# Kernel tuning notes

Hardware: AMD Instinct MI355X
Metric: run time of the kernel (lower is better)

The kernel has to match this reference:

```python
import jax, jax.numpy as jnp
import numpy as np

V, E, H, S, L = 32000, 512, 1024, 512, 256


def _cell(x, h, c, Wih, Whh, bih, bhh):
    # PyTorch LSTM cell, gate order i, f, g, o
    gates = Wih @ x + bih + Whh @ h + bhh
    i, f, g, o = jnp.split(gates, 4)
    c2 = jax.nn.sigmoid(f) * c + jax.nn.sigmoid(i) * jnp.tanh(g)
    h2 = jax.nn.sigmoid(o) * jnp.tanh(c2)
    return h2, c2


def setup_inputs() -> dict:
    key = jax.random.key(0)
    ks = jax.random.split(key, 24)
    s = 0.03  # ~1/sqrt(H), like torch LSTM default init scale
    def n(k, shape, scale=s):
        return jax.random.normal(k, shape, dtype=jnp.float32) * scale
    return {
        "x": jax.random.randint(ks[0], (S,), 0, V),
        "y": jax.random.randint(ks[1], (L,), 0, V),
        "emb": n(ks[2], (V, E)),
        "enc_Wih0": n(ks[3], (4 * H, E)), "enc_Whh0": n(ks[4], (4 * H, H)),
        "enc_bih0": n(ks[5], (4 * H,)), "enc_bhh0": n(ks[6], (4 * H,)),
        "enc_Wih1": n(ks[7], (4 * H, H)), "enc_Whh1": n(ks[8], (4 * H, H)),
        "enc_bih1": n(ks[9], (4 * H,)), "enc_bhh1": n(ks[10], (4 * H,)),
        "enc_fcW": n(ks[11], (H, H)), "enc_fcb": n(ks[12], (H,)),
        # decoder input is the raw token id as a float; scale its input weight
        # by ~1/V so gate pre-activations stay O(1)
        "dec_Wih0": n(ks[13], (4 * H, 1), 1.0 / V), "dec_Whh0": n(ks[14], (4 * H, H)),
        "dec_bih0": n(ks[15], (4 * H,)), "dec_bhh0": n(ks[16], (4 * H,)),
        "dec_Wih1": n(ks[17], (4 * H, H)), "dec_Whh1": n(ks[18], (4 * H, H)),
        "dec_bih1": n(ks[19], (4 * H,)), "dec_bhh1": n(ks[20], (4 * H,)),
        "dec_fcW": n(ks[21], (V, H)), "dec_fcb": n(ks[22], (V,)),
    }


def reference(x, y, emb, enc_Wih0, enc_Whh0, enc_bih0, enc_bhh0,
              enc_Wih1, enc_Whh1, enc_bih1, enc_bhh1, enc_fcW, enc_fcb,
              dec_Wih0, dec_Whh0, dec_bih0, dec_bhh0,
              dec_Wih1, dec_Whh1, dec_bih1, dec_bhh1, dec_fcW, dec_fcb):
    h_dim = enc_Whh0.shape[1]
    vocab = dec_fcW.shape[0]

    # ---- Encoder: 2-layer LSTM over the noisy sequence, batch=1 ----
    emb_seq = emb[x]  # [S, E]

    def enc_step(carry, e_t):
        h0, c0, h1, c1 = carry
        h0, c0 = _cell(e_t, h0, c0, enc_Wih0, enc_Whh0, enc_bih0, enc_bhh0)
        h1, c1 = _cell(h0, h1, c1, enc_Wih1, enc_Whh1, enc_bih1, enc_bhh1)
        return (h0, c0, h1, c1), None

    z = jnp.zeros((h_dim,), jnp.float32)
    (_, _, h1, _), _ = jax.lax.scan(enc_step, (z, z, z, z), emb_seq)
    lat = jax.nn.relu(enc_fcW @ h1 + enc_fcb)       # [H] (latent == hidden)
    h_s0 = jnp.stack([lat, lat])                    # replicated across layers

    # ---- Decoder: free-running greedy decode (tfr=0.0) ----
    # Faithful quirk: each step re-initializes the cell state to the hidden
    # state (original passes (h_s_enc, h_s_enc) every call).
    def dec_step(carry, _):
        x_f, h = carry
        h0n, _ = _cell(jnp.reshape(x_f, (1,)), h[0], h[0],
                       dec_Wih0, dec_Whh0, dec_bih0, dec_bhh0)
        h1n, _ = _cell(h0n, h[1], h[1],
                       dec_Wih1, dec_Whh1, dec_bih1, dec_bhh1)
        logits = dec_fcW @ h1n + dec_fcb            # [V]
        x_next = jnp.argmax(logits).astype(jnp.float32)
        return (x_next, jnp.stack([h0n, h1n])), logits

    x0 = y[0].astype(jnp.float32)
    _, logits_seq = jax.lax.scan(dec_step, (x0, h_s0), None, length=y.shape[0] - 1)
    # outputs[0] stays zeros, as in the original
    return jnp.concatenate([jnp.zeros((1, vocab), jnp.float32), logits_seq], axis=0)
```

## Files before the change

kernel.cpp:

```cpp
#include <hip/hip_runtime.h>
#include <hip/hip_bf16.h>

typedef unsigned short u16;
typedef unsigned int   u32;

#define NB    256
#define NT    512
#define HD    1024
#define G4    4096
#define VOCAB 32000
#define EDIM  512
#define SLEN  512
#define RPB   (VOCAB / NB)

__device__ __forceinline__ float bflo(u32 u){ union{u32 i; float f;} v; v.i = u << 16; return v.f; }
__device__ __forceinline__ float bfhi(u32 u){ union{u32 i; float f;} v; v.i = u & 0xffff0000u; return v.f; }
__device__ __forceinline__ float bf1(u16 u){ union{u32 i; float f;} v; v.i = ((u32)u) << 16; return v.f; }
__device__ __forceinline__ u16 f2bf(float f){
    union{float f; u32 i;} v; v.f = f;
    u32 x = v.i;
    u32 r = (x + 0x7fffu + ((x >> 16) & 1u)) >> 16;
    return (u16)r;
}

__device__ __forceinline__ float sigm(float x){ return 1.f / (1.f + __expf(-x)); }
__device__ __forceinline__ float tanh_f(float x){ float e = __expf(2.f * x); return 1.f - 2.f / (e + 1.f); }

__device__ __forceinline__ float wave_sum(float v){
#pragma unroll
    for (int off = 32; off > 0; off >>= 1) v += __shfl_xor(v, off, 64);
    return v;
}

__device__ __forceinline__ float dot16bf(uint4 a, uint4 b, const float* h){
    float s = 0.f;
    s = fmaf(bflo(a.x), h[0],  s); s = fmaf(bfhi(a.x), h[1],  s);
    s = fmaf(bflo(a.y), h[2],  s); s = fmaf(bfhi(a.y), h[3],  s);
    s = fmaf(bflo(a.z), h[4],  s); s = fmaf(bfhi(a.z), h[5],  s);
    s = fmaf(bflo(a.w), h[6],  s); s = fmaf(bfhi(a.w), h[7],  s);
    s = fmaf(bflo(b.x), h[8],  s); s = fmaf(bfhi(b.x), h[9],  s);
    s = fmaf(bflo(b.y), h[10], s); s = fmaf(bfhi(b.y), h[11], s);
    s = fmaf(bflo(b.z), h[12], s); s = fmaf(bfhi(b.z), h[13], s);
    s = fmaf(bflo(b.w), h[14], s); s = fmaf(bfhi(b.w), h[15], s);
    return s;
}

__device__ __forceinline__ void load16(const float* src, int lane, float* d){
    const float4* p = (const float4*)(src + (lane << 4));
    float4 a = p[0], b = p[1], c = p[2], e = p[3];
    d[0]=a.x; d[1]=a.y; d[2]=a.z; d[3]=a.w;
    d[4]=b.x; d[5]=b.y; d[6]=b.z; d[7]=b.w;
    d[8]=c.x; d[9]=c.y; d[10]=c.z; d[11]=c.w;
    d[12]=e.x; d[13]=e.y; d[14]=e.z; d[15]=e.w;
}

struct TBF {
    static __device__ __forceinline__ float g(const void* p, int i){ return bf1(((const u16*)p)[i]); }
    static __device__ __forceinline__ const void* rp(const void* p, size_t eoff){ return (const void*)((const u16*)p + eoff); }
    static __device__ __forceinline__ float dot1024(const void* pr, const float* h, int lane){
        const u16* row = (const u16*)pr;
        const uint4* p = (const uint4*)(row + ((size_t)lane << 4));
        uint4 a = p[0], b = p[1];
        return dot16bf(a, b, h);
    }
    static __device__ __forceinline__ float dot512(const void* pr, const float* h8, int lane){
        const u16* row = (const u16*)pr;
        uint4 a = *((const uint4*)(row + ((size_t)lane << 3)));
        float s = 0.f;
        s = fmaf(bflo(a.x), h8[0], s); s = fmaf(bfhi(a.x), h8[1], s);
        s = fmaf(bflo(a.y), h8[2], s); s = fmaf(bfhi(a.y), h8[3], s);
        s = fmaf(bflo(a.z), h8[4], s); s = fmaf(bfhi(a.z), h8[5], s);
        s = fmaf(bflo(a.w), h8[6], s); s = fmaf(bfhi(a.w), h8[7], s);
        return s;
    }
    static __device__ __forceinline__ void vec8(const void* pr, int lane, float* d){
        const u16* src = (const u16*)pr;
        uint4 a = *((const uint4*)(src + ((size_t)lane << 3)));
        d[0]=bflo(a.x); d[1]=bfhi(a.x); d[2]=bflo(a.y); d[3]=bfhi(a.y);
        d[4]=bflo(a.z); d[5]=bfhi(a.z); d[6]=bflo(a.w); d[7]=bfhi(a.w);
    }
    static __device__ __forceinline__ void store(void* o, size_t i, float v){ ((u16*)o)[i] = f2bf(v); }
    static __device__ __forceinline__ void zero(void* o, size_t i){ ((u16*)o)[i] = 0; }
};

struct TF32 {
    static __device__ __forceinline__ float g(const void* p, int i){ return ((const float*)p)[i]; }
    static __device__ __forceinline__ const void* rp(const void* p, size_t eoff){ return (const void*)((const float*)p + eoff); }
    static __device__ __forceinline__ float dot1024(const void* pr, const float* h, int lane){
        const float4* p = (const float4*)((const float*)pr + ((size_t)lane << 4));
        float4 a = p[0], b = p[1], c = p[2], e = p[3];
        float s = 0.f;
        s = fmaf(a.x, h[0],  s); s = fmaf(a.y, h[1],  s); s = fmaf(a.z, h[2],  s); s = fmaf(a.w, h[3],  s);
        s = fmaf(b.x, h[4],  s); s = fmaf(b.y, h[5],  s); s = fmaf(b.z, h[6],  s); s = fmaf(b.w, h[7],  s);
        s = fmaf(c.x, h[8],  s); s = fmaf(c.y, h[9],  s); s = fmaf(c.z, h[10], s); s = fmaf(c.w, h[11], s);
        s = fmaf(e.x, h[12], s); s = fmaf(e.y, h[13], s); s = fmaf(e.z, h[14], s); s = fmaf(e.w, h[15], s);
        return s;
    }
    static __device__ __forceinline__ float dot512(const void* pr, const float* h8, int lane){
        const float4* p = (const float4*)((const float*)pr + ((size_t)lane << 3));
        float4 a = p[0], b = p[1];
        float s = 0.f;
        s = fmaf(a.x, h8[0], s); s = fmaf(a.y, h8[1], s); s = fmaf(a.z, h8[2], s); s = fmaf(a.w, h8[3], s);
        s = fmaf(b.x, h8[4], s); s = fmaf(b.y, h8[5], s); s = fmaf(b.z, h8[6], s); s = fmaf(b.w, h8[7], s);
        return s;
    }
    static __device__ __forceinline__ void vec8(const void* pr, int lane, float* d){
        const float4* p = (const float4*)((const float*)pr + ((size_t)lane << 3));
        float4 a = p[0], b = p[1];
        d[0]=a.x; d[1]=a.y; d[2]=a.z; d[3]=a.w;
        d[4]=b.x; d[5]=b.y; d[6]=b.z; d[7]=b.w;
    }
    static __device__ __forceinline__ void store(void* o, size_t i, float v){ ((float*)o)[i] = v; }
    static __device__ __forceinline__ void zero(void* o, size_t i){ ((float*)o)[i] = 0.f; }
};

__device__ __forceinline__ void grid_barrier(u32* bar, u32 tgen, int bid){
    __syncthreads();
    if (threadIdx.x == 0){
        __builtin_amdgcn_fence(__ATOMIC_RELEASE, "agent");
        u32 a = __hip_atomic_fetch_add(&bar[(bid & 7) * 32], 1u,
                                       __ATOMIC_RELAXED, __HIP_MEMORY_SCOPE_AGENT);
        if ((a % 32u) == 31u){
            u32 m = __hip_atomic_fetch_add(&bar[256], 1u,
                                           __ATOMIC_RELAXED, __HIP_MEMORY_SCOPE_AGENT);
            if ((m % 8u) == 7u)
                __hip_atomic_store(&bar[288], tgen, __ATOMIC_RELAXED, __HIP_MEMORY_SCOPE_AGENT);
        }
        while (__hip_atomic_load(&bar[288], __ATOMIC_RELAXED, __HIP_MEMORY_SCOPE_AGENT) < tgen)
            __builtin_amdgcn_s_sleep(1);
        __builtin_amdgcn_fence(__ATOMIC_ACQUIRE, "agent");
    }
    __syncthreads();
}

__global__ void ws_init(u32* ws){
    int i = threadIdx.x + blockIdx.x * blockDim.x;
    if (i < 1024) ws[i] = 0u;
}

__global__ void dtype_probe(const u16* emb, u32* ws){
    __shared__ int sh[4];
    int tid = threadIdx.x;
    int bad = 0;
    for (int i = tid; i < 2048; i += 256){
        u32 e = ((u32)emb[i] >> 7) & 0xFFu;
        if (e >= 0x82u) bad++;
    }
#pragma unroll
    for (int off = 32; off > 0; off >>= 1) bad += __shfl_xor(bad, off, 64);
    if ((tid & 63) == 0) sh[tid >> 6] = bad;
    __syncthreads();
    if (tid == 0){
        int t = sh[0] + sh[1] + sh[2] + sh[3];
        ws[512] = (t > 8) ? 1u : 0u;
    }
}

template<class W, u32 WANT>
__global__ __launch_bounds__(NT) void dae_main(
    const int* __restrict__ xs, const int* __restrict__ ys,
    const void* __restrict__ emb,
    const void* __restrict__ eWih0, const void* __restrict__ eWhh0,
    const void* __restrict__ ebih0, const void* __restrict__ ebhh0,
    const void* __restrict__ eWih1, const void* __restrict__ eWhh1,
    const void* __restrict__ ebih1, const void* __restrict__ ebhh1,
    const void* __restrict__ efcW,  const void* __restrict__ efcb,
    const void* __restrict__ dWih0, const void* __restrict__ dWhh0,
    const void* __restrict__ dbih0, const void* __restrict__ dbhh0,
    const void* __restrict__ dWih1, const void* __restrict__ dWhh1,
    const void* __restrict__ dbih1, const void* __restrict__ dbhh1,
    const void* __restrict__ dfcW,  const void* __restrict__ dfcb,
    void* __restrict__ out, u32* __restrict__ ws)
{
    if (__hip_atomic_load(&ws[512], __ATOMIC_RELAXED, __HIP_MEMORY_SCOPE_AGENT) != WANT) return;

    const int tid  = threadIdx.x;
    const int bid  = blockIdx.x;
    const int lane = tid & 63;
    const int wave = tid >> 6;

    __shared__ __align__(16) float h0s[HD];
    __shared__ __align__(16) float h1s[HD];
    __shared__ float redmax[8];
    __shared__ int   redidx[8];
    __shared__ float xf_sh;

    u32*   bar  = ws;
    float* G0   = (float*)(ws + 1024);
    float* G1   = G0 + 2 * G4;
    float* M0   = G1 + 2 * G4;
    float* Fv   = M0 + 2 * G4;
    float* bmax = Fv + HD;
    int*   bidxv= (int*)(bmax + NB);

    u32 phase = 0;
    float c0r[2] = {0.f, 0.f};
    float c1r[2] = {0.f, 0.f};

    for (int i = tid; i < HD; i += NT){ h0s[i] = 0.f; h1s[i] = 0.f; }
    for (int i = tid; i < RPB; i += NT) W::zero(out, (size_t)bid * RPB + i);

    {
        int tok = xs[0];
        float er[8];
        W::vec8(W::rp(emb, (size_t)tok * EDIM), lane, er);
        const int rb = bid * 16 + wave * 2;
#pragma unroll
        for (int i = 0; i < 2; ++i){
            int r = rb + i;
            float s = W::dot512(W::rp(eWih0, (size_t)r * EDIM), er, lane);
            s = wave_sum(s);
            if (lane == 0) G0[r] = s + W::g(ebih0, r) + W::g(ebhh0, r);
        }
    }
    grid_barrier(bar, ++phase, bid);

    for (int t = 0; t < SLEN; ++t){
        const int cur = t & 1, nxt = cur ^ 1;
        if (t >= 1){
            const float* Gg = G1 + nxt * G4;
#pragma unroll
            for (int i = 0; i < 2; ++i){
                int r = tid * 2 + i;
                float ig = Gg[r], fg = Gg[r + HD], gg = Gg[r + 2*HD], og = Gg[r + 3*HD];
                float c = sigm(fg) * c1r[i] + sigm(ig) * tanh_f(gg);
                c1r[i] = c;
                h1s[r] = sigm(og) * tanh_f(c);
            }
        }
        {
            const float* Gg = G0 + cur * G4;
#pragma unroll
            for (int i = 0; i < 2; ++i){
                int r = tid * 2 + i;
                float ig = Gg[r], fg = Gg[r + HD], gg = Gg[r + 2*HD], og = Gg[r + 3*HD];
                float c = sigm(fg) * c0r[i] + sigm(ig) * tanh_f(gg);
                c0r[i] = c;
                h0s[r] = sigm(og) * tanh_f(c);
            }
        }
        __syncthreads();
        float h0r[16], h1r[16];
        load16(h0s, lane, h0r);
        load16(h1s, lane, h1r);
        const int rb = bid * 16 + wave * 2;
        if (t < SLEN - 1){
            int tok = xs[t + 1];
            float er[8];
            W::vec8(W::rp(emb, (size_t)tok * EDIM), lane, er);
#pragma unroll
            for (int i = 0; i < 2; ++i){
                int r = rb + i;
                float s = W::dot1024(W::rp(eWhh0, (size_t)r * HD), h0r, lane)
                        + W::dot512(W::rp(eWih0, (size_t)r * EDIM), er, lane);
                s = wave_sum(s);
                if (lane == 0) G0[nxt * G4 + r] = s + W::g(ebih0, r) + W::g(ebhh0, r);
            }
        }
#pragma unroll
        for (int i = 0; i < 2; ++i){
            int r = rb + i;
            float s = W::dot1024(W::rp(eWih1, (size_t)r * HD), h0r, lane)
                    + W::dot1024(W::rp(eWhh1, (size_t)r * HD), h1r, lane);
            s = wave_sum(s);
            if (lane == 0) G1[cur * G4 + r] = s + W::g(ebih1, r) + W::g(ebhh1, r);
        }
        grid_barrier(bar, ++phase, bid);
    }

    {
        const float* Gg = G1 + ((SLEN - 1) & 1) * G4;
#pragma unroll
        for (int i = 0; i < 2; ++i){
            int r = tid * 2 + i;
            float ig = Gg[r], fg = Gg[r + HD], gg = Gg[r + 2*HD], og = Gg[r + 3*HD];
            float c = sigm(fg) * c1r[i] + sigm(ig) * tanh_f(gg);
            c1r[i] = c;
            h1s[r] = sigm(og) * tanh_f(c);
        }
        __syncthreads();
        float h1r[16];
        load16(h1s, lane, h1r);
        if (wave < 4){
            int r = bid * 4 + wave;
            float s = W::dot1024(W::rp(efcW, (size_t)r * HD), h1r, lane);
            s = wave_sum(s);
            if (lane == 0) Fv[r] = s + W::g(efcb, r);
        }
        grid_barrier(bar, ++phase, bid);
    }

    {
        for (int i = tid; i < HD; i += NT){
            float v = Fv[i]; v = v > 0.f ? v : 0.f;
            h0s[i] = v; h1s[i] = v;
        }
        __syncthreads();
        float h0r[16];
        load16(h0s, lane, h0r);
        const int rb = bid * 16 + wave * 2;
#pragma unroll
        for (int i = 0; i < 2; ++i){
            int r = rb + i;
            float s = W::dot1024(W::rp(dWhh0, (size_t)r * HD), h0r, lane);
            s = wave_sum(s);
            if (lane == 0) M0[G4 + r] = s + W::g(dbih0, r) + W::g(dbhh0, r);
        }
        grid_barrier(bar, ++phase, bid);
    }

    for (int t = 1; t < 256; ++t){
        float xf;
        if (t == 1){
            xf = (float)ys[0];
        } else {
            if (wave == 0){
                float m = bmax[lane]; int mi = bidxv[lane];
#pragma unroll
                for (int j = 64; j < NB; j += 64){
                    float m2 = bmax[lane + j]; int i2 = bidxv[lane + j];
                    if (m2 > m || (m2 == m && i2 < mi)){ m = m2; mi = i2; }
                }
#pragma unroll
                for (int off = 32; off > 0; off >>= 1){
                    float m2 = __shfl_xor(m, off, 64);
                    int   i2 = __shfl_xor(mi, off, 64);
                    if (m2 > m || (m2 == m && i2 < mi)){ m = m2; mi = i2; }
                }
                if (lane == 0) xf_sh = (float)mi;
            }
            __syncthreads();
            xf = xf_sh;
        }
        {
            const float* Gg = M0 + (t & 1) * G4;
#pragma unroll
            for (int i = 0; i < 2; ++i){
                int r = tid * 2 + i;
                float ig = Gg[r]        + xf * W::g(dWih0, r);
                float fg = Gg[r + HD]   + xf * W::g(dWih0, r + HD);
                float gg = Gg[r + 2*HD] + xf * W::g(dWih0, r + 2*HD);
                float og = Gg[r + 3*HD] + xf * W::g(dWih0, r + 3*HD);
                float cp = h0s[r];
                float c  = sigm(fg) * cp + sigm(ig) * tanh_f(gg);
                h0s[r]   = sigm(og) * tanh_f(c);
            }
        }
        __syncthreads();
        {
            float h0r[16], h1r[16];
            load16(h0s, lane, h0r);
            load16(h1s, lane, h1r);
            const int rb = bid * 16 + wave * 2;
#pragma unroll
            for (int i = 0; i < 2; ++i){
                int r = rb + i;
                float s1 = W::dot1024(W::rp(dWih1, (size_t)r * HD), h0r, lane)
                         + W::dot1024(W::rp(dWhh1, (size_t)r * HD), h1r, lane);
                s1 = wave_sum(s1);
                if (lane == 0) G1[(t & 1) * G4 + r] = s1 + W::g(dbih1, r) + W::g(dbhh1, r);
                float s0 = W::dot1024(W::rp(dWhh0, (size_t)r * HD), h0r, lane);
                s0 = wave_sum(s0);
                if (lane == 0) M0[((t + 1) & 1) * G4 + r] = s0 + W::g(dbih0, r) + W::g(dbhh0, r);
            }
        }
        grid_barrier(bar, ++phase, bid);

        {
            const float* Gg = G1 + (t & 1) * G4;
#pragma unroll
            for (int i = 0; i < 2; ++i){
                int r = tid * 2 + i;
                float ig = Gg[r], fg = Gg[r + HD], gg = Gg[r + 2*HD], og = Gg[r + 3*HD];
                float cp = h1s[r];
                float c  = sigm(fg) * cp + sigm(ig) * tanh_f(gg);
                h1s[r]   = sigm(og) * tanh_f(c);
            }
        }
        __syncthreads();
        {
            float h1r[16];
            load16(h1s, lane, h1r);
            float wmax = -3.4e38f; int wmi = 0x7fffffff;
            for (int i = wave; i < RPB; i += 8){
                int r = bid * RPB + i;
                float s = W::dot1024(W::rp(dfcW, (size_t)r * HD), h1r, lane);
                s = wave_sum(s) + W::g(dfcb, r);
                if (lane == 0) W::store(out, (size_t)t * VOCAB + r, s);
                if (s > wmax){ wmax = s; wmi = r; }
            }
            if (lane == 0){ redmax[wave] = wmax; redidx[wave] = wmi; }
        }
        __syncthreads();
        if (tid == 0){
            float m = redmax[0]; int mi = redidx[0];
#pragma unroll
            for (int w = 1; w < 8; ++w){
                if (redmax[w] > m || (redmax[w] == m && redidx[w] < mi)){ m = redmax[w]; mi = redidx[w]; }
            }
            bmax[bid] = m; bidxv[bid] = mi;
        }
        grid_barrier(bar, ++phase, bid);
    }
}

extern "C" void kernel_launch(void* const* d_in, const int* in_sizes, int n_in,
                              void* d_out, int out_size, void* d_ws, size_t ws_size,
                              hipStream_t stream) {
    const int* xs = (const int*)d_in[0];
    const int* ys = (const int*)d_in[1];
    u32* ws = (u32*)d_ws;

    ws_init<<<4, 256, 0, stream>>>(ws);
    dtype_probe<<<1, 256, 0, stream>>>((const u16*)d_in[2], ws);

    dae_main<TBF, 0u><<<NB, NT, 0, stream>>>(
        xs, ys, d_in[2],
        d_in[3], d_in[4], d_in[5], d_in[6], d_in[7], d_in[8], d_in[9], d_in[10],
        d_in[11], d_in[12],
        d_in[13], d_in[14], d_in[15], d_in[16], d_in[17], d_in[18], d_in[19], d_in[20],
        d_in[21], d_in[22],
        d_out, ws);
    dae_main<TF32, 1u><<<NB, NT, 0, stream>>>(
        xs, ys, d_in[2],
        d_in[3], d_in[4], d_in[5], d_in[6], d_in[7], d_in[8], d_in[9], d_in[10],
        d_in[11], d_in[12],
        d_in[13], d_in[14], d_in[15], d_in[16], d_in[17], d_in[18], d_in[19], d_in[20],
        d_in[21], d_in[22],
        d_out, ws);
}
```

Baseline: 16.08 ms.

## Replace barrier acquire fence with agent-scope atomic loads and unroll vocab projection

Drops the acquire fence in the grid barrier, which invalidates caches. All cross-block shared buffers (gate pre-activations, latent, argmax partials) are instead read and written with relaxed agent-scope atomic loads and stores so they stay coherent. The vocab projection loop is also unrolled by two rows per wave to overlap two dot products. Correctness now relies on every cross-block access going through the atomic helpers. A missed access, or compiler reordering without the fence, could read stale data.

```diff
diff --git a/kernel.cpp b/kernel.cpp
--- a/kernel.cpp
+++ b/kernel.cpp
@@ -25,6 +25,19 @@
 
 __device__ __forceinline__ float sigm(float x){ return 1.f / (1.f + __expf(-x)); }
 __device__ __forceinline__ float tanh_f(float x){ float e = __expf(2.f * x); return 1.f - 2.f / (e + 1.f); }
+
+__device__ __forceinline__ float gldf(const float* p){
+    return __hip_atomic_load(p, __ATOMIC_RELAXED, __HIP_MEMORY_SCOPE_AGENT);
+}
+__device__ __forceinline__ void gstf(float* p, float v){
+    __hip_atomic_store(p, v, __ATOMIC_RELAXED, __HIP_MEMORY_SCOPE_AGENT);
+}
+__device__ __forceinline__ int gldi(const int* p){
+    return __hip_atomic_load(p, __ATOMIC_RELAXED, __HIP_MEMORY_SCOPE_AGENT);
+}
+__device__ __forceinline__ void gsti(int* p, int v){
+    __hip_atomic_store(p, v, __ATOMIC_RELAXED, __HIP_MEMORY_SCOPE_AGENT);
+}
 
 __device__ __forceinline__ float wave_sum(float v){
 #pragma unroll
@@ -128,7 +141,7 @@
         }
         while (__hip_atomic_load(&bar[288], __ATOMIC_RELAXED, __HIP_MEMORY_SCOPE_AGENT) < tgen)
             __builtin_amdgcn_s_sleep(1);
-        __builtin_amdgcn_fence(__ATOMIC_ACQUIRE, "agent");
+        asm volatile("" ::: "memory");
     }
     __syncthreads();
 }
@@ -210,7 +223,7 @@
             int r = rb + i;
             float s = W::dot512(W::rp(eWih0, (size_t)r * EDIM), er, lane);
             s = wave_sum(s);
-            if (lane == 0) G0[r] = s + W::g(ebih0, r) + W::g(ebhh0, r);
+            if (lane == 0) gstf(&G0[r], s + W::g(ebih0, r) + W::g(ebhh0, r));
         }
     }
     grid_barrier(bar, ++phase, bid);
@@ -222,7 +235,8 @@
 #pragma unroll
             for (int i = 0; i < 2; ++i){
                 int r = tid * 2 + i;
-                float ig = Gg[r], fg = Gg[r + HD], gg = Gg[r + 2*HD], og = Gg[r + 3*HD];
+                float ig = gldf(&Gg[r]),        fg = gldf(&Gg[r + HD]);
+                float gg = gldf(&Gg[r + 2*HD]), og = gldf(&Gg[r + 3*HD]);
                 float c = sigm(fg) * c1r[i] + sigm(ig) * tanh_f(gg);
                 c1r[i] = c;
                 h1s[r] = sigm(og) * tanh_f(c);
@@ -233,7 +247,8 @@
 #pragma unroll
             for (int i = 0; i < 2; ++i){
                 int r = tid * 2 + i;
-                float ig = Gg[r], fg = Gg[r + HD], gg = Gg[r + 2*HD], og = Gg[r + 3*HD];
+                float ig = gldf(&Gg[r]),        fg = gldf(&Gg[r + HD]);
+                float gg = gldf(&Gg[r + 2*HD]), og = gldf(&Gg[r + 3*HD]);
                 float c = sigm(fg) * c0r[i] + sigm(ig) * tanh_f(gg);
                 c0r[i] = c;
                 h0s[r] = sigm(og) * tanh_f(c);
@@ -254,7 +269,7 @@
                 float s = W::dot1024(W::rp(eWhh0, (size_t)r * HD), h0r, lane)
                         + W::dot512(W::rp(eWih0, (size_t)r * EDIM), er, lane);
                 s = wave_sum(s);
-                if (lane == 0) G0[nxt * G4 + r] = s + W::g(ebih0, r) + W::g(ebhh0, r);
+                if (lane == 0) gstf(&G0[nxt * G4 + r], s + W::g(ebih0, r) + W::g(ebhh0, r));
             }
         }
 #pragma unroll
@@ -263,7 +278,7 @@
             float s = W::dot1024(W::rp(eWih1, (size_t)r * HD), h0r, lane)
                     + W::dot1024(W::rp(eWhh1, (size_t)r * HD), h1r, lane);
             s = wave_sum(s);
-            if (lane == 0) G1[cur * G4 + r] = s + W::g(ebih1, r) + W::g(ebhh1, r);
+            if (lane == 0) gstf(&G1[cur * G4 + r], s + W::g(ebih1, r) + W::g(ebhh1, r));
         }
         grid_barrier(bar, ++phase, bid);
     }
@@ -273,7 +288,8 @@
 #pragma unroll
         for (int i = 0; i < 2; ++i){
             int r = tid * 2 + i;
-            float ig = Gg[r], fg = Gg[r + HD], gg = Gg[r + 2*HD], og = Gg[r + 3*HD];
+            float ig = gldf(&Gg[r]),        fg = gldf(&Gg[r + HD]);
+            float gg = gldf(&Gg[r + 2*HD]), og = gldf(&Gg[r + 3*HD]);
             float c = sigm(fg) * c1r[i] + sigm(ig) * tanh_f(gg);
             c1r[i] = c;
             h1s[r] = sigm(og) * tanh_f(c);
@@ -285,14 +301,14 @@
             int r = bid * 4 + wave;
             float s = W::dot1024(W::rp(efcW, (size_t)r * HD), h1r, lane);
             s = wave_sum(s);
-            if (lane == 0) Fv[r] = s + W::g(efcb, r);
+            if (lane == 0) gstf(&Fv[r], s + W::g(efcb, r));
         }
         grid_barrier(bar, ++phase, bid);
     }
 
     {
         for (int i = tid; i < HD; i += NT){
-            float v = Fv[i]; v = v > 0.f ? v : 0.f;
+            float v = gldf(&Fv[i]); v = v > 0.f ? v : 0.f;
             h0s[i] = v; h1s[i] = v;
         }
         __syncthreads();
@@ -304,7 +320,7 @@
             int r = rb + i;
             float s = W::dot1024(W::rp(dWhh0, (size_t)r * HD), h0r, lane);
             s = wave_sum(s);
-            if (lane == 0) M0[G4 + r] = s + W::g(dbih0, r) + W::g(dbhh0, r);
+            if (lane == 0) gstf(&M0[G4 + r], s + W::g(dbih0, r) + W::g(dbhh0, r));
         }
         grid_barrier(bar, ++phase, bid);
     }
@@ -315,10 +331,10 @@
             xf = (float)ys[0];
         } else {
             if (wave == 0){
-                float m = bmax[lane]; int mi = bidxv[lane];
+                float m = gldf(&bmax[lane]); int mi = gldi(&bidxv[lane]);
 #pragma unroll
                 for (int j = 64; j < NB; j += 64){
-                    float m2 = bmax[lane + j]; int i2 = bidxv[lane + j];
+                    float m2 = gldf(&bmax[lane + j]); int i2 = gldi(&bidxv[lane + j]);
                     if (m2 > m || (m2 == m && i2 < mi)){ m = m2; mi = i2; }
                 }
 #pragma unroll
@@ -337,10 +353,10 @@
 #pragma unroll
             for (int i = 0; i < 2; ++i){
                 int r = tid * 2 + i;
-                float ig = Gg[r]        + xf * W::g(dWih0, r);
-                float fg = Gg[r + HD]   + xf * W::g(dWih0, r + HD);
-                float gg = Gg[r + 2*HD] + xf * W::g(dWih0, r + 2*HD);
-                float og = Gg[r + 3*HD] + xf * W::g(dWih0, r + 3*HD);
+                float ig = gldf(&Gg[r])        + xf * W::g(dWih0, r);
+                float fg = gldf(&Gg[r + HD])   + xf * W::g(dWih0, r + HD);
+                float gg = gldf(&Gg[r + 2*HD]) + xf * W::g(dWih0, r + 2*HD);
+                float og = gldf(&Gg[r + 3*HD]) + xf * W::g(dWih0, r + 3*HD);
                 float cp = h0s[r];
                 float c  = sigm(fg) * cp + sigm(ig) * tanh_f(gg);
                 h0s[r]   = sigm(og) * tanh_f(c);
@@ -358,10 +374,10 @@
                 float s1 = W::dot1024(W::rp(dWih1, (size_t)r * HD), h0r, lane)
                          + W::dot1024(W::rp(dWhh1, (size_t)r * HD), h1r, lane);
                 s1 = wave_sum(s1);
-                if (lane == 0) G1[(t & 1) * G4 + r] = s1 + W::g(dbih1, r) + W::g(dbhh1, r);
+                if (lane == 0) gstf(&G1[(t & 1) * G4 + r], s1 + W::g(dbih1, r) + W::g(dbhh1, r));
                 float s0 = W::dot1024(W::rp(dWhh0, (size_t)r * HD), h0r, lane);
                 s0 = wave_sum(s0);
-                if (lane == 0) M0[((t + 1) & 1) * G4 + r] = s0 + W::g(dbih0, r) + W::g(dbhh0, r);
+                if (lane == 0) gstf(&M0[((t + 1) & 1) * G4 + r], s0 + W::g(dbih0, r) + W::g(dbhh0, r));
             }
         }
         grid_barrier(bar, ++phase, bid);
@@ -371,7 +387,8 @@
 #pragma unroll
             for (int i = 0; i < 2; ++i){
                 int r = tid * 2 + i;
-                float ig = Gg[r], fg = Gg[r + HD], gg = Gg[r + 2*HD], og = Gg[r + 3*HD];
+                float ig = gldf(&Gg[r]),        fg = gldf(&Gg[r + HD]);
+                float gg = gldf(&Gg[r + 2*HD]), og = gldf(&Gg[r + 3*HD]);
                 float cp = h1s[r];
                 float c  = sigm(fg) * cp + sigm(ig) * tanh_f(gg);
                 h1s[r]   = sigm(og) * tanh_f(c);
@@ -382,7 +399,21 @@
             float h1r[16];
             load16(h1s, lane, h1r);
             float wmax = -3.4e38f; int wmi = 0x7fffffff;
-            for (int i = wave; i < RPB; i += 8){
+            int i = wave;
+            for (; i + 8 < RPB; i += 16){
+                int r1 = bid * RPB + i, r2 = r1 + 8;
+                float s1 = W::dot1024(W::rp(dfcW, (size_t)r1 * HD), h1r, lane);
+                float s2 = W::dot1024(W::rp(dfcW, (size_t)r2 * HD), h1r, lane);
+                s1 = wave_sum(s1); s2 = wave_sum(s2);
+                s1 += W::g(dfcb, r1); s2 += W::g(dfcb, r2);
+                if (lane == 0){
+                    W::store(out, (size_t)t * VOCAB + r1, s1);
+                    W::store(out, (size_t)t * VOCAB + r2, s2);
+                }
+                if (s1 > wmax){ wmax = s1; wmi = r1; }
+                if (s2 > wmax){ wmax = s2; wmi = r2; }
+            }
+            if (i < RPB){
                 int r = bid * RPB + i;
                 float s = W::dot1024(W::rp(dfcW, (size_t)r * HD), h1r, lane);
                 s = wave_sum(s) + W::g(dfcb, r);
@@ -398,7 +429,7 @@
             for (int w = 1; w < 8; ++w){
                 if (redmax[w] > m || (redmax[w] == m && redidx[w] < mi)){ m = redmax[w]; mi = redidx[w]; }
             }
-            bmax[bid] = m; bidxv[bid] = mi;
+            gstf(&bmax[bid], m); gsti(&bidxv[bid], mi);
         }
         grid_barrier(bar, ++phase, bid);
     }
```

After: 13.58 ms. -15.5%, faster.
